# Optimization experiments

Hardware: AMD Instinct MI355X
Metric: run time of the kernel (lower is better)

## Reference

```python
import jax, jax.numpy as jnp
import numpy as np

# Fixed causal graph: 32 endo nodes, each with a private 16-dim exogenous parent.
# Nodes 0..3 are roots (no endo parents); node i>=4 has endo parents {i-4..i-1}.
N_NODES = 32
ENDO = 16      # endogenous features per node
EXO = 16       # exogenous features per node
HID = 64       # hidden width (module default hidden_features=[64,64])
N_ROOTS = 4
N_PAR = 4      # endo parents for non-root nodes
IN_ROOT = EXO                      # 16
IN_INNER = N_PAR * ENDO + EXO      # 80
BATCH = 32768


def _init(key, shape, fan_in):
    return jax.random.normal(key, shape, jnp.float32) * (1.0 / np.sqrt(fan_in))


def setup_inputs() -> dict:
    key = jax.random.key(0)
    ks = jax.random.split(key, 13)
    n_in = N_NODES - N_ROOTS
    return {
        "u": jax.random.normal(ks[0], (BATCH, N_NODES * EXO), jnp.float32),
        # stacked root MLPs: [n_roots, in, out]
        "w_r1": _init(ks[1], (N_ROOTS, IN_ROOT, HID), IN_ROOT),
        "b_r1": jnp.zeros((N_ROOTS, HID), jnp.float32),
        "w_r2": _init(ks[2], (N_ROOTS, HID, HID), HID),
        "b_r2": jnp.zeros((N_ROOTS, HID), jnp.float32),
        "w_r3": _init(ks[3], (N_ROOTS, HID, ENDO), HID),
        "b_r3": jnp.zeros((N_ROOTS, ENDO), jnp.float32),
        # stacked inner MLPs: [n_inner, in, out]
        "w_i1": _init(ks[4], (n_in, IN_INNER, HID), IN_INNER),
        "b_i1": jnp.zeros((n_in, HID), jnp.float32),
        "w_i2": _init(ks[5], (n_in, HID, HID), HID),
        "b_i2": jnp.zeros((n_in, HID), jnp.float32),
        "w_i3": _init(ks[6], (n_in, HID, ENDO), HID),
        "b_i3": jnp.zeros((n_in, ENDO), jnp.float32),
    }


def _mlp(x, w1, b1, w2, b2, w3, b3):
    h = jax.nn.relu(x @ w1 + b1)
    h = jax.nn.relu(h @ w2 + b2)
    return h @ w3 + b3


def reference(u, w_r1, b_r1, w_r2, b_r2, w_r3, b_r3,
              w_i1, b_i1, w_i2, b_i2, w_i3, b_i3):
    B = u.shape[0]
    U = u.reshape(B, N_NODES, EXO)  # per-node exogenous inputs
    # Root nodes: no endo parents, vectorized over the 4 roots.
    h = jax.nn.relu(jnp.einsum("bni,nio->bno", U[:, :N_ROOTS], w_r1) + b_r1)
    h = jax.nn.relu(jnp.einsum("bnh,nho->bno", h, w_r2) + b_r2)
    root_v = jnp.einsum("bnh,nhd->bnd", h, w_r3) + b_r3  # [B, 4, ENDO]
    V = [root_v[:, i] for i in range(N_ROOTS)]
    # Non-root nodes in topological order: gather thresholded parents -> MLP.
    for i in range(N_ROOTS, N_NODES):
        j = i - N_ROOTS
        parents = jnp.concatenate(
            [(V[p] > 0.5).astype(u.dtype) for p in range(i - N_PAR, i)], axis=-1)
        inp = jnp.concatenate([parents, U[:, i]], axis=-1)  # [B, 80]
        V.append(_mlp(inp, w_i1[j], b_i1[j], w_i2[j], b_i2[j], w_i3[j], b_i3[j]))
    # forward() uses soft=True, T/W_T/W_E=None -> E is the raw logits, batched.
    return jnp.concatenate(V, axis=-1)  # [B, N_NODES*ENDO]
```

## Files before the change

kernel.cpp:

```cpp
#include <hip/hip_runtime.h>


#define BT 64

typedef __attribute__((ext_vector_type(8))) short bf16x8;
typedef __attribute__((ext_vector_type(4))) float f32x4;
#define MFMA16 __builtin_amdgcn_mfma_f32_16x16x32_bf16

#define NODE_STRIDE 33792
#define W1_SPLIT    6144
#define W2_OFF      18432
#define W2_SPLIT    4096
#define W3_OFF      30720
#define W3_SPLIT    1024

__device__ inline unsigned short bf16_rne(float x) {
    unsigned u = __float_as_uint(x);
    u += 0x7fffu + ((u >> 16) & 1u);
    return (unsigned short)(u >> 16);
}
__device__ inline float bf16_tof(unsigned short h) {
    return __uint_as_float(((unsigned)h) << 16);
}
__device__ inline void split3(float x, unsigned short& h, unsigned short& m,
                              unsigned short& l) {
    h = bf16_rne(x);
    float r = x - bf16_tof(h);
    m = bf16_rne(r);
    float r2 = r - bf16_tof(m);
    l = bf16_rne(r2);
}

__device__ inline unsigned cvt_pk_bf16(float a, float b) {
    unsigned d;
    asm("v_cvt_pk_bf16_f32 %0, %1, %2" : "=v"(d) : "v"(a), "v"(b));
    return d;
}
__device__ inline void split3_pair(float a, float b,
                                   unsigned& h, unsigned& m, unsigned& l) {
    h = cvt_pk_bf16(a, b);
    float ra = a - __uint_as_float(h << 16);
    float rb = b - __uint_as_float(h & 0xffff0000u);
    m = cvt_pk_bf16(ra, rb);
    float sa = ra - __uint_as_float(m << 16);
    float sb = rb - __uint_as_float(m & 0xffff0000u);
    l = cvt_pk_bf16(sa, sb);
}

__device__ inline int hswz(int e, int feat) {
    return (feat & 7) | ((((feat >> 3) ^ e) & 7) << 3);
}

#define PER_NODE_ITEMS (64 * 96 + 64 * 64 + 16 * 64)

__global__ void prep_weights(const float* __restrict__ w_r1,
                             const float* __restrict__ w_r2,
                             const float* __restrict__ w_r3,
                             const float* __restrict__ w_i1,
                             const float* __restrict__ w_i2,
                             const float* __restrict__ w_i3,
                             unsigned short* __restrict__ ws) {
    int tid = blockIdx.x * 256 + threadIdx.x;
    if (tid >= 32 * PER_NODE_ITEMS) return;
    int node = tid / PER_NODE_ITEMS;
    int r = tid - node * PER_NODE_ITEMS;
    int off, stride;
    float wv = 0.0f;
    if (r < 6144) {
        int n = r / 96, k = r - n * 96;
        if (k < 64) {
            wv = (node >= 4) ? w_i1[((node - 4) * 80 + k) * 64 + n] : 0.0f;
        } else if (k < 80) {
            wv = (node < 4) ? w_r1[(node * 16 + (k - 64)) * 64 + n]
                            : w_i1[((node - 4) * 80 + k) * 64 + n];
        }
        off = n * 96 + k; stride = W1_SPLIT;
    } else if (r < 10240) {
        int r2 = r - 6144;
        int n = r2 >> 6, k = r2 & 63;
        wv = (node < 4) ? w_r2[(node * 64 + k) * 64 + n]
                        : w_i2[((node - 4) * 64 + k) * 64 + n];
        off = W2_OFF + n * 64 + k; stride = W2_SPLIT;
    } else {
        int r3 = r - 10240;
        int n = r3 >> 6, k = r3 & 63;
        wv = (node < 4) ? w_r3[(node * 64 + k) * 16 + n]
                        : w_i3[((node - 4) * 64 + k) * 16 + n];
        off = W3_OFF + n * 64 + k; stride = W3_SPLIT;
    }
    unsigned short h, m, l;
    split3(wv, h, m, l);
    unsigned short* base = ws + node * NODE_STRIDE;
    base[off] = h;
    base[off + stride] = m;
    base[off + 2 * stride] = l;
}

__global__ __launch_bounds__(256, 2) void ncm_mfma(
    const float* __restrict__ u,
    const unsigned short* __restrict__ ws,
    const float* __restrict__ b_r1, const float* __restrict__ b_r2,
    const float* __restrict__ b_r3, const float* __restrict__ b_i1,
    const float* __restrict__ b_i2, const float* __restrict__ b_i3,
    float* __restrict__ out)
{
    __shared__ __align__(16) unsigned short ring[4][64][24];
    __shared__ __align__(16) unsigned short xu[3][64][40];
    __shared__ __align__(16) unsigned short h1s[3][64][64];
    __shared__ __align__(16) unsigned short h2s[3][64][64];

    const int tid = threadIdx.x;
    const int l   = tid & 63;
    const int w   = tid >> 6;
    const int lr  = l & 15;
    const int lq  = l >> 4;
    const int n1  = 16 * w + lr;

    const long eg = (long)blockIdx.x * BT;
    const float* u_blk = u + eg * 512;


    for (int i = 0; i < 32; ++i) {
        __syncthreads();

        {
            float4 uv = *(const float4*)(u_blk + (long)l * 512 + i * 16 + w * 4);
            unsigned hP0, mP0, lP0, hP1, mP1, lP1;
            split3_pair(uv.x, uv.y, hP0, mP0, lP0);
            split3_pair(uv.z, uv.w, hP1, mP1, lP1);
            *(uint2*)&xu[0][l][4 * w] = make_uint2(hP0, hP1);
            *(uint2*)&xu[1][l][4 * w] = make_uint2(mP0, mP1);
            *(uint2*)&xu[2][l][4 * w] = make_uint2(lP0, lP1);
        }
        __syncthreads();

        const unsigned short* Wn = ws + i * NODE_STRIDE;
        f32x4 acc[4] = {{0,0,0,0},{0,0,0,0},{0,0,0,0},{0,0,0,0}};

        if (i >= 4) {
            #pragma unroll
            for (int k0 = 0; k0 < 64; k0 += 32) {
                const int f = k0 + lq * 8;
                const int slot = (i + (f >> 4)) & 3;
                const unsigned short* wp = Wn + n1 * 96 + f;
                bf16x8 wb0 = *(const bf16x8*)(wp);
                bf16x8 wb1 = *(const bf16x8*)(wp + W1_SPLIT);
                bf16x8 wb2 = *(const bf16x8*)(wp + 2 * W1_SPLIT);
                #pragma unroll
                for (int m = 0; m < 4; ++m) {
                    bf16x8 ab = *(const bf16x8*)&ring[slot][m * 16 + lr][f & 15];
                    acc[m] = MFMA16(wb0, ab, acc[m], 0, 0, 0);
                    acc[m] = MFMA16(wb1, ab, acc[m], 0, 0, 0);
                    acc[m] = MFMA16(wb2, ab, acc[m], 0, 0, 0);
                }
            }
        }
        {
            const unsigned short* wp = Wn + n1 * 96 + 64 + lq * 8;
            bf16x8 wb0 = *(const bf16x8*)(wp);
            bf16x8 wb1 = *(const bf16x8*)(wp + W1_SPLIT);
            bf16x8 wb2 = *(const bf16x8*)(wp + 2 * W1_SPLIT);
            #pragma unroll
            for (int m = 0; m < 4; ++m) {
                bf16x8 a0 = {}, a1 = {}, a2 = {};
                if (lq < 2) {
                    const int e = m * 16 + lr;
                    a0 = *(const bf16x8*)&xu[0][e][lq * 8];
                    a1 = *(const bf16x8*)&xu[1][e][lq * 8];
                    a2 = *(const bf16x8*)&xu[2][e][lq * 8];
                }
                acc[m] = MFMA16(wb0, a0, acc[m], 0, 0, 0);
                acc[m] = MFMA16(wb1, a0, acc[m], 0, 0, 0);
                acc[m] = MFMA16(wb2, a0, acc[m], 0, 0, 0);
                acc[m] = MFMA16(wb0, a1, acc[m], 0, 0, 0);
                acc[m] = MFMA16(wb1, a1, acc[m], 0, 0, 0);
                acc[m] = MFMA16(wb2, a1, acc[m], 0, 0, 0);
                acc[m] = MFMA16(wb0, a2, acc[m], 0, 0, 0);
                acc[m] = MFMA16(wb1, a2, acc[m], 0, 0, 0);
            }
        }
        {
            const float* B1 = (i < 4) ? (b_r1 + i * 64) : (b_i1 + (i - 4) * 64);
            float4 bv = *(const float4*)(B1 + 16 * w + 4 * lq);
            const int fo = 16 * w + 4 * lq;
            #pragma unroll
            for (int m = 0; m < 4; ++m) {
                const int e = m * 16 + lr;
                float v0 = fmaxf(acc[m][0] + bv.x, 0.0f);
                float v1 = fmaxf(acc[m][1] + bv.y, 0.0f);
                float v2 = fmaxf(acc[m][2] + bv.z, 0.0f);
                float v3 = fmaxf(acc[m][3] + bv.w, 0.0f);
                unsigned hP0, mP0, lP0, hP1, mP1, lP1;
                split3_pair(v0, v1, hP0, mP0, lP0);
                split3_pair(v2, v3, hP1, mP1, lP1);
                const int o = hswz(e, fo);
                *(uint2*)&h1s[0][e][o] = make_uint2(hP0, hP1);
                *(uint2*)&h1s[1][e][o] = make_uint2(mP0, mP1);
                *(uint2*)&h1s[2][e][o] = make_uint2(lP0, lP1);
            }
        }
        __syncthreads();

        #pragma unroll
        for (int m = 0; m < 4; ++m) acc[m] = (f32x4){0, 0, 0, 0};
        {
            const unsigned short* W2 = Wn + W2_OFF;
            #pragma unroll
            for (int k0 = 0; k0 < 64; k0 += 32) {
                const int f = k0 + lq * 8;
                const unsigned short* wp = W2 + n1 * 64 + f;
                bf16x8 wb0 = *(const bf16x8*)(wp);
                bf16x8 wb1 = *(const bf16x8*)(wp + W2_SPLIT);
                bf16x8 wb2 = *(const bf16x8*)(wp + 2 * W2_SPLIT);
                #pragma unroll
                for (int m = 0; m < 4; ++m) {
                    const int e = m * 16 + lr;
                    const int o = hswz(e, f);
                    bf16x8 a0 = *(const bf16x8*)&h1s[0][e][o];
                    bf16x8 a1 = *(const bf16x8*)&h1s[1][e][o];
                    bf16x8 a2 = *(const bf16x8*)&h1s[2][e][o];
                    acc[m] = MFMA16(wb0, a0, acc[m], 0, 0, 0);
                    acc[m] = MFMA16(wb1, a0, acc[m], 0, 0, 0);
                    acc[m] = MFMA16(wb2, a0, acc[m], 0, 0, 0);
                    acc[m] = MFMA16(wb0, a1, acc[m], 0, 0, 0);
                    acc[m] = MFMA16(wb1, a1, acc[m], 0, 0, 0);
                    acc[m] = MFMA16(wb2, a1, acc[m], 0, 0, 0);
                    acc[m] = MFMA16(wb0, a2, acc[m], 0, 0, 0);
                    acc[m] = MFMA16(wb1, a2, acc[m], 0, 0, 0);
                }
            }
        }
        {
            const float* B2 = (i < 4) ? (b_r2 + i * 64) : (b_i2 + (i - 4) * 64);
            float4 bv = *(const float4*)(B2 + 16 * w + 4 * lq);
            const int fo = 16 * w + 4 * lq;
            #pragma unroll
            for (int m = 0; m < 4; ++m) {
                const int e = m * 16 + lr;
                float v0 = fmaxf(acc[m][0] + bv.x, 0.0f);
                float v1 = fmaxf(acc[m][1] + bv.y, 0.0f);
                float v2 = fmaxf(acc[m][2] + bv.z, 0.0f);
                float v3 = fmaxf(acc[m][3] + bv.w, 0.0f);
                unsigned hP0, mP0, lP0, hP1, mP1, lP1;
                split3_pair(v0, v1, hP0, mP0, lP0);
                split3_pair(v2, v3, hP1, mP1, lP1);
                const int o = hswz(e, fo);
                *(uint2*)&h2s[0][e][o] = make_uint2(hP0, hP1);
                *(uint2*)&h2s[1][e][o] = make_uint2(mP0, mP1);
                *(uint2*)&h2s[2][e][o] = make_uint2(lP0, lP1);
            }
        }
        __syncthreads();

        {
            f32x4 c3 = {0, 0, 0, 0};
            const unsigned short* W3 = Wn + W3_OFF;
            const int e = 16 * w + lr;
            #pragma unroll
            for (int k0 = 0; k0 < 64; k0 += 32) {
                const int f = k0 + lq * 8;
                const unsigned short* wp = W3 + lr * 64 + f;
                bf16x8 wb0 = *(const bf16x8*)(wp);
                bf16x8 wb1 = *(const bf16x8*)(wp + W3_SPLIT);
                bf16x8 wb2 = *(const bf16x8*)(wp + 2 * W3_SPLIT);
                const int o = hswz(e, f);
                bf16x8 a0 = *(const bf16x8*)&h2s[0][e][o];
                bf16x8 a1 = *(const bf16x8*)&h2s[1][e][o];
                bf16x8 a2 = *(const bf16x8*)&h2s[2][e][o];
                c3 = MFMA16(wb0, a0, c3, 0, 0, 0);
                c3 = MFMA16(wb1, a0, c3, 0, 0, 0);
                c3 = MFMA16(wb2, a0, c3, 0, 0, 0);
                c3 = MFMA16(wb0, a1, c3, 0, 0, 0);
                c3 = MFMA16(wb1, a1, c3, 0, 0, 0);
                c3 = MFMA16(wb2, a1, c3, 0, 0, 0);
                c3 = MFMA16(wb0, a2, c3, 0, 0, 0);
                c3 = MFMA16(wb1, a2, c3, 0, 0, 0);
            }
            const float* B3 = (i < 4) ? (b_r3 + i * 16) : (b_i3 + (i - 4) * 16);
            float4 bv = *(const float4*)(B3 + 4 * lq);
            float v0 = c3[0] + bv.x;
            float v1 = c3[1] + bv.y;
            float v2 = c3[2] + bv.z;
            float v3 = c3[3] + bv.w;
            *(float4*)(out + (eg + e) * 512 + i * 16 + 4 * lq) =
                make_float4(v0, v1, v2, v3);
            const int slot = i & 3;
            unsigned r0 = (v0 > 0.5f ? 0x3F80u : 0u) |
                          ((v1 > 0.5f ? 0x3F80u : 0u) << 16);
            unsigned r1 = (v2 > 0.5f ? 0x3F80u : 0u) |
                          ((v3 > 0.5f ? 0x3F80u : 0u) << 16);
            *(uint2*)&ring[slot][e][4 * lq] = make_uint2(r0, r1);
        }
    }
}

extern "C" void kernel_launch(void* const* d_in, const int* in_sizes, int n_in,
                              void* d_out, int out_size, void* d_ws, size_t ws_size,
                              hipStream_t stream) {
    const float* u    = (const float*)d_in[0];
    const float* w_r1 = (const float*)d_in[1];
    const float* b_r1 = (const float*)d_in[2];
    const float* w_r2 = (const float*)d_in[3];
    const float* b_r2 = (const float*)d_in[4];
    const float* w_r3 = (const float*)d_in[5];
    const float* b_r3 = (const float*)d_in[6];
    const float* w_i1 = (const float*)d_in[7];
    const float* b_i1 = (const float*)d_in[8];
    const float* w_i2 = (const float*)d_in[9];
    const float* b_i2 = (const float*)d_in[10];
    const float* w_i3 = (const float*)d_in[11];
    const float* b_i3 = (const float*)d_in[12];
    float* out = (float*)d_out;
    unsigned short* ws = (unsigned short*)d_ws;

    prep_weights<<<dim3((32 * PER_NODE_ITEMS) / 256), dim3(256), 0, stream>>>(
        w_r1, w_r2, w_r3, w_i1, w_i2, w_i3, ws);

    ncm_mfma<<<dim3(512), dim3(256), 0, stream>>>(
        u, ws, b_r1, b_r2, b_r3, b_i1, b_i2, b_i3, out);
}
```

Baseline: 324.0 us.

## Prefetch next-node weights and inputs into registers across MLP stages

Moves weight fragment loads into register arrays and issues them one stage ahead, so next-node layer-1 and layer-2 weights load while the current node's later layers compute. The next node's exogenous input is also prefetched and split into LDS mid-iteration. Barriers are reduced from four to three per node and replaced by a custom lgkmcnt-only wait plus s_barrier. This hides global load latency at the cost of more VGPRs, which may pressure occupancy at 2 blocks per CU. Relying only on lgkmcnt for the barrier is correct only if every LDS write is ordered by it.

```diff
diff --git a/kernel.cpp b/kernel.cpp
--- a/kernel.cpp
+++ b/kernel.cpp
@@ -49,6 +49,10 @@
 
 __device__ inline int hswz(int e, int feat) {
     return (feat & 7) | ((((feat >> 3) ^ e) & 7) << 3);
+}
+
+__device__ inline void bar_lgkm() {
+    asm volatile("s_waitcnt lgkmcnt(0)\n\ts_barrier" ::: "memory");
 }
 
 #define PER_NODE_ITEMS (64 * 96 + 64 * 64 + 16 * 64)
@@ -96,6 +100,51 @@
     base[off + 2 * stride] = l;
 }
 
+#define LOAD_W1(nn) do {                                                      \
+    const unsigned short* Wb_ = ws + (long)(nn) * NODE_STRIDE + n1 * 96;      \
+    _Pragma("unroll") for (int g_ = 0; g_ < 2; ++g_) {                        \
+        const unsigned short* wp_ = Wb_ + g_ * 32 + lq * 8;                   \
+        w1f[g_ * 3 + 0] = *(const bf16x8*)(wp_);                              \
+        w1f[g_ * 3 + 1] = *(const bf16x8*)(wp_ + W1_SPLIT);                   \
+        w1f[g_ * 3 + 2] = *(const bf16x8*)(wp_ + 2 * W1_SPLIT);               \
+    }                                                                         \
+    const unsigned short* we_ = Wb_ + 64 + lq * 8;                            \
+    w1f[6] = *(const bf16x8*)(we_);                                           \
+    w1f[7] = *(const bf16x8*)(we_ + W1_SPLIT);                                \
+    w1f[8] = *(const bf16x8*)(we_ + 2 * W1_SPLIT);                            \
+} while (0)
+
+#define LOAD_W2(nn) do {                                                      \
+    const unsigned short* Wb_ =                                               \
+        ws + (long)(nn) * NODE_STRIDE + W2_OFF + n1 * 64;                     \
+    _Pragma("unroll") for (int g_ = 0; g_ < 2; ++g_) {                        \
+        const unsigned short* wp_ = Wb_ + g_ * 32 + lq * 8;                   \
+        w2f[g_ * 3 + 0] = *(const bf16x8*)(wp_);                              \
+        w2f[g_ * 3 + 1] = *(const bf16x8*)(wp_ + W2_SPLIT);                   \
+        w2f[g_ * 3 + 2] = *(const bf16x8*)(wp_ + 2 * W2_SPLIT);               \
+    }                                                                         \
+} while (0)
+
+#define LOAD_W3(nn) do {                                                      \
+    const unsigned short* Wb_ =                                               \
+        ws + (long)(nn) * NODE_STRIDE + W3_OFF + lr * 64;                     \
+    _Pragma("unroll") for (int g_ = 0; g_ < 2; ++g_) {                        \
+        const unsigned short* wp_ = Wb_ + g_ * 32 + lq * 8;                   \
+        w3f[g_ * 3 + 0] = *(const bf16x8*)(wp_);                              \
+        w3f[g_ * 3 + 1] = *(const bf16x8*)(wp_ + W3_SPLIT);                   \
+        w3f[g_ * 3 + 2] = *(const bf16x8*)(wp_ + 2 * W3_SPLIT);               \
+    }                                                                         \
+} while (0)
+
+#define STAGE_XU(uv) do {                                                     \
+    unsigned hS0_, mS0_, lS0_, hS1_, mS1_, lS1_;                              \
+    split3_pair((uv).x, (uv).y, hS0_, mS0_, lS0_);                            \
+    split3_pair((uv).z, (uv).w, hS1_, mS1_, lS1_);                            \
+    *(uint2*)&xu[0][l][4 * w] = make_uint2(hS0_, hS1_);                       \
+    *(uint2*)&xu[1][l][4 * w] = make_uint2(mS0_, mS1_);                       \
+    *(uint2*)&xu[2][l][4 * w] = make_uint2(lS0_, lS1_);                       \
+} while (0)
+
 __global__ __launch_bounds__(256, 2) void ncm_mfma(
     const float* __restrict__ u,
     const unsigned short* __restrict__ ws,
@@ -119,47 +168,40 @@
     const long eg = (long)blockIdx.x * BT;
     const float* u_blk = u + eg * 512;
 
+    bf16x8 w1f[9], w2f[6], w3f[6];
+
+    LOAD_W1(0);
+    LOAD_W2(0);
+    {
+        float4 uv = *(const float4*)(u_blk + (long)l * 512 + w * 4);
+        STAGE_XU(uv);
+    }
+    bar_lgkm();
 
     for (int i = 0; i < 32; ++i) {
-        __syncthreads();
-
-        {
-            float4 uv = *(const float4*)(u_blk + (long)l * 512 + i * 16 + w * 4);
-            unsigned hP0, mP0, lP0, hP1, mP1, lP1;
-            split3_pair(uv.x, uv.y, hP0, mP0, lP0);
-            split3_pair(uv.z, uv.w, hP1, mP1, lP1);
-            *(uint2*)&xu[0][l][4 * w] = make_uint2(hP0, hP1);
-            *(uint2*)&xu[1][l][4 * w] = make_uint2(mP0, mP1);
-            *(uint2*)&xu[2][l][4 * w] = make_uint2(lP0, lP1);
-        }
-        __syncthreads();
-
-        const unsigned short* Wn = ws + i * NODE_STRIDE;
+        const int nn = (i < 31) ? i + 1 : 31;
         f32x4 acc[4] = {{0,0,0,0},{0,0,0,0},{0,0,0,0},{0,0,0,0}};
 
+        LOAD_W3(i);
+        float4 uN;
+        if (i < 31)
+            uN = *(const float4*)(u_blk + (long)l * 512 + nn * 16 + w * 4);
+
         if (i >= 4) {
             #pragma unroll
-            for (int k0 = 0; k0 < 64; k0 += 32) {
-                const int f = k0 + lq * 8;
+            for (int g = 0; g < 2; ++g) {
+                const int f = g * 32 + lq * 8;
                 const int slot = (i + (f >> 4)) & 3;
-                const unsigned short* wp = Wn + n1 * 96 + f;
-                bf16x8 wb0 = *(const bf16x8*)(wp);
-                bf16x8 wb1 = *(const bf16x8*)(wp + W1_SPLIT);
-                bf16x8 wb2 = *(const bf16x8*)(wp + 2 * W1_SPLIT);
                 #pragma unroll
                 for (int m = 0; m < 4; ++m) {
                     bf16x8 ab = *(const bf16x8*)&ring[slot][m * 16 + lr][f & 15];
-                    acc[m] = MFMA16(wb0, ab, acc[m], 0, 0, 0);
-                    acc[m] = MFMA16(wb1, ab, acc[m], 0, 0, 0);
-                    acc[m] = MFMA16(wb2, ab, acc[m], 0, 0, 0);
+                    acc[m] = MFMA16(w1f[g * 3 + 0], ab, acc[m], 0, 0, 0);
+                    acc[m] = MFMA16(w1f[g * 3 + 1], ab, acc[m], 0, 0, 0);
+                    acc[m] = MFMA16(w1f[g * 3 + 2], ab, acc[m], 0, 0, 0);
                 }
             }
         }
         {
-            const unsigned short* wp = Wn + n1 * 96 + 64 + lq * 8;
-            bf16x8 wb0 = *(const bf16x8*)(wp);
-            bf16x8 wb1 = *(const bf16x8*)(wp + W1_SPLIT);
-            bf16x8 wb2 = *(const bf16x8*)(wp + 2 * W1_SPLIT);
             #pragma unroll
             for (int m = 0; m < 4; ++m) {
                 bf16x8 a0 = {}, a1 = {}, a2 = {};
@@ -169,14 +211,14 @@
                     a1 = *(const bf16x8*)&xu[1][e][lq * 8];
                     a2 = *(const bf16x8*)&xu[2][e][lq * 8];
                 }
-                acc[m] = MFMA16(wb0, a0, acc[m], 0, 0, 0);
-                acc[m] = MFMA16(wb1, a0, acc[m], 0, 0, 0);
-                acc[m] = MFMA16(wb2, a0, acc[m], 0, 0, 0);
-                acc[m] = MFMA16(wb0, a1, acc[m], 0, 0, 0);
-                acc[m] = MFMA16(wb1, a1, acc[m], 0, 0, 0);
-                acc[m] = MFMA16(wb2, a1, acc[m], 0, 0, 0);
-                acc[m] = MFMA16(wb0, a2, acc[m], 0, 0, 0);
-                acc[m] = MFMA16(wb1, a2, acc[m], 0, 0, 0);
+                acc[m] = MFMA16(w1f[6], a0, acc[m], 0, 0, 0);
+                acc[m] = MFMA16(w1f[7], a0, acc[m], 0, 0, 0);
+                acc[m] = MFMA16(w1f[8], a0, acc[m], 0, 0, 0);
+                acc[m] = MFMA16(w1f[6], a1, acc[m], 0, 0, 0);
+                acc[m] = MFMA16(w1f[7], a1, acc[m], 0, 0, 0);
+                acc[m] = MFMA16(w1f[8], a1, acc[m], 0, 0, 0);
+                acc[m] = MFMA16(w1f[6], a2, acc[m], 0, 0, 0);
+                acc[m] = MFMA16(w1f[7], a2, acc[m], 0, 0, 0);
             }
         }
         {
@@ -199,19 +241,17 @@
                 *(uint2*)&h1s[2][e][o] = make_uint2(lP0, lP1);
             }
         }
-        __syncthreads();
+        bar_lgkm();
+
+        LOAD_W1(nn);
+        if (i < 31) STAGE_XU(uN);
 
         #pragma unroll
         for (int m = 0; m < 4; ++m) acc[m] = (f32x4){0, 0, 0, 0};
         {
-            const unsigned short* W2 = Wn + W2_OFF;
-            #pragma unroll
-            for (int k0 = 0; k0 < 64; k0 += 32) {
-                const int f = k0 + lq * 8;
-                const unsigned short* wp = W2 + n1 * 64 + f;
-                bf16x8 wb0 = *(const bf16x8*)(wp);
-                bf16x8 wb1 = *(const bf16x8*)(wp + W2_SPLIT);
-                bf16x8 wb2 = *(const bf16x8*)(wp + 2 * W2_SPLIT);
+            #pragma unroll
+            for (int g = 0; g < 2; ++g) {
+                const int f = g * 32 + lq * 8;
                 #pragma unroll
                 for (int m = 0; m < 4; ++m) {
                     const int e = m * 16 + lr;
@@ -219,14 +259,14 @@
                     bf16x8 a0 = *(const bf16x8*)&h1s[0][e][o];
                     bf16x8 a1 = *(const bf16x8*)&h1s[1][e][o];
                     bf16x8 a2 = *(const bf16x8*)&h1s[2][e][o];
-                    acc[m] = MFMA16(wb0, a0, acc[m], 0, 0, 0);
-                    acc[m] = MFMA16(wb1, a0, acc[m], 0, 0, 0);
-                    acc[m] = MFMA16(wb2, a0, acc[m], 0, 0, 0);
-                    acc[m] = MFMA16(wb0, a1, acc[m], 0, 0, 0);
-                    acc[m] = MFMA16(wb1, a1, acc[m], 0, 0, 0);
-                    acc[m] = MFMA16(wb2, a1, acc[m], 0, 0, 0);
-                    acc[m] = MFMA16(wb0, a2, acc[m], 0, 0, 0);
-                    acc[m] = MFMA16(wb1, a2, acc[m], 0, 0, 0);
+                    acc[m] = MFMA16(w2f[g * 3 + 0], a0, acc[m], 0, 0, 0);
+                    acc[m] = MFMA16(w2f[g * 3 + 1], a0, acc[m], 0, 0, 0);
+                    acc[m] = MFMA16(w2f[g * 3 + 2], a0, acc[m], 0, 0, 0);
+                    acc[m] = MFMA16(w2f[g * 3 + 0], a1, acc[m], 0, 0, 0);
+                    acc[m] = MFMA16(w2f[g * 3 + 1], a1, acc[m], 0, 0, 0);
+                    acc[m] = MFMA16(w2f[g * 3 + 2], a1, acc[m], 0, 0, 0);
+                    acc[m] = MFMA16(w2f[g * 3 + 0], a2, acc[m], 0, 0, 0);
+                    acc[m] = MFMA16(w2f[g * 3 + 1], a2, acc[m], 0, 0, 0);
                 }
             }
         }
@@ -250,31 +290,27 @@
                 *(uint2*)&h2s[2][e][o] = make_uint2(lP0, lP1);
             }
         }
-        __syncthreads();
-
+        bar_lgkm();
+
+        LOAD_W2(nn);
         {
             f32x4 c3 = {0, 0, 0, 0};
-            const unsigned short* W3 = Wn + W3_OFF;
             const int e = 16 * w + lr;
             #pragma unroll
-            for (int k0 = 0; k0 < 64; k0 += 32) {
-                const int f = k0 + lq * 8;
-                const unsigned short* wp = W3 + lr * 64 + f;
-                bf16x8 wb0 = *(const bf16x8*)(wp);
-                bf16x8 wb1 = *(const bf16x8*)(wp + W3_SPLIT);
-                bf16x8 wb2 = *(const bf16x8*)(wp + 2 * W3_SPLIT);
+            for (int g = 0; g < 2; ++g) {
+                const int f = g * 32 + lq * 8;
                 const int o = hswz(e, f);
                 bf16x8 a0 = *(const bf16x8*)&h2s[0][e][o];
                 bf16x8 a1 = *(const bf16x8*)&h2s[1][e][o];
                 bf16x8 a2 = *(const bf16x8*)&h2s[2][e][o];
-                c3 = MFMA16(wb0, a0, c3, 0, 0, 0);
-                c3 = MFMA16(wb1, a0, c3, 0, 0, 0);
-                c3 = MFMA16(wb2, a0, c3, 0, 0, 0);
-                c3 = MFMA16(wb0, a1, c3, 0, 0, 0);
-                c3 = MFMA16(wb1, a1, c3, 0, 0, 0);
-                c3 = MFMA16(wb2, a1, c3, 0, 0, 0);
-                c3 = MFMA16(wb0, a2, c3, 0, 0, 0);
-                c3 = MFMA16(wb1, a2, c3, 0, 0, 0);
+                c3 = MFMA16(w3f[g * 3 + 0], a0, c3, 0, 0, 0);
+                c3 = MFMA16(w3f[g * 3 + 1], a0, c3, 0, 0, 0);
+                c3 = MFMA16(w3f[g * 3 + 2], a0, c3, 0, 0, 0);
+                c3 = MFMA16(w3f[g * 3 + 0], a1, c3, 0, 0, 0);
+                c3 = MFMA16(w3f[g * 3 + 1], a1, c3, 0, 0, 0);
+                c3 = MFMA16(w3f[g * 3 + 2], a1, c3, 0, 0, 0);
+                c3 = MFMA16(w3f[g * 3 + 0], a2, c3, 0, 0, 0);
+                c3 = MFMA16(w3f[g * 3 + 1], a2, c3, 0, 0, 0);
             }
             const float* B3 = (i < 4) ? (b_r3 + i * 16) : (b_i3 + (i - 4) * 16);
             float4 bv = *(const float4*)(B3 + 4 * lq);
@@ -291,6 +327,7 @@
                           ((v3 > 0.5f ? 0x3F80u : 0u) << 16);
             *(uint2*)&ring[slot][e][4 * lq] = make_uint2(r0, r1);
         }
+        bar_lgkm();
     }
 }
 
```

After: 284.4 us. -12.2%, faster.
